# Kernel tuning notes

Hardware: AMD Instinct MI355X
Metric: run time of the kernel (lower is better)

Reference implementation:

```python
import jax, jax.numpy as jnp
import numpy as np

GWIDTH2 = 0.3  # Gaussian bandwidth squared
PNORM = 2


def setup_inputs() -> dict:
    key = jax.random.key(0)
    k1, k2 = jax.random.split(key)
    b, c, h, w = 16, 3, 256, 256
    npro = 32
    x = jax.random.uniform(k1, (b, c, h, w), dtype=jnp.float32)  # pixel values in [0,1]
    P = jax.random.uniform(k2, (npro, c), dtype=jnp.float32)     # p x c prototype pixels
    return {"x": x, "P": P}


def reference(x, P):
    # x: (b, c, h, w); P: (p, c)
    b, c, h, w = x.shape
    # broadcast difference -> (b, p, c, h, w); pnorm=2 distance over channels
    diff = x[:, None, :, :, :] - P[None, :, :, None, None]
    normsp = jnp.sum(diff ** PNORM, axis=2) ** (1.0 / PNORM)  # (b, p, h, w)
    expo = jnp.exp(-normsp / (2.0 * GWIDTH2))
    Y = jnp.sum(expo, axis=(2, 3))  # (b, p)
    return Y / (h * w)
```

## Files before the change

### kernel.cpp

```cpp
#include <hip/hip_runtime.h>


#define NPRO    32
#define HW      65536
#define THREADS 256
#define BPB     32
#define KITER   (HW / (BPB * THREADS * 4))

__global__ __launch_bounds__(THREADS) void soft_count_kernel(
    const float* __restrict__ x, const float* __restrict__ P,
    float* __restrict__ out)
{
    __shared__ float sP[NPRO * 3];
    __shared__ float sred[4][NPRO];

    const int tid = threadIdx.x;
    if (tid < NPRO * 3) sP[tid] = P[tid];
    __syncthreads();

    const int b   = blockIdx.x / BPB;
    const int blk = blockIdx.x % BPB;

    const float* xr = x + (size_t)b * 3 * HW;
    const float* xg = xr + HW;
    const float* xb = xr + 2 * HW;

    float acc[NPRO];
#pragma unroll
    for (int p = 0; p < NPRO; ++p) acc[p] = 0.0f;

    const int base = blk * (THREADS * 4 * KITER);

#pragma unroll
    for (int k = 0; k < KITER; ++k) {
        const int idx = base + k * (THREADS * 4) + tid * 4;
        const float4 r4 = *(const float4*)(xr + idx);
        const float4 g4 = *(const float4*)(xg + idx);
        const float4 b4 = *(const float4*)(xb + idx);
        const float rr[4] = {r4.x, r4.y, r4.z, r4.w};
        const float gg[4] = {g4.x, g4.y, g4.z, g4.w};
        const float bb[4] = {b4.x, b4.y, b4.z, b4.w};

#pragma unroll
        for (int p = 0; p < NPRO; ++p) {
            const float p0 = sP[p * 3 + 0];
            const float p1 = sP[p * 3 + 1];
            const float p2 = sP[p * 3 + 2];
            float s = 0.0f;
#pragma unroll
            for (int j = 0; j < 4; ++j) {
                const float d0 = rr[j] - p0;
                const float d1 = gg[j] - p1;
                const float d2 = bb[j] - p2;
                const float n2 = d0 * d0 + d1 * d1 + d2 * d2;
                const float nrm = sqrtf(n2);
                s += __expf(nrm * (-1.0f / 0.6f));
            }
            acc[p] += s;
        }
    }

    const int lane = tid & 63;
    const int wv   = tid >> 6;
#pragma unroll
    for (int p = 0; p < NPRO; ++p) {
        float v = acc[p];
#pragma unroll
        for (int off = 32; off >= 1; off >>= 1)
            v += __shfl_down(v, off, 64);
        if (lane == 0) sred[wv][p] = v;
    }
    __syncthreads();

    if (tid < NPRO) {
        const float v = sred[0][tid] + sred[1][tid] + sred[2][tid] + sred[3][tid];
        atomicAdd(&out[b * NPRO + tid], v * (1.0f / (float)HW));
    }
}

__global__ void zero_out_kernel(float* out, int n) {
    const int i = blockIdx.x * blockDim.x + threadIdx.x;
    if (i < n) out[i] = 0.0f;
}

extern "C" void kernel_launch(void* const* d_in, const int* in_sizes, int n_in,
                              void* d_out, int out_size, void* d_ws, size_t ws_size,
                              hipStream_t stream) {
    const float* x = (const float*)d_in[0];
    const float* P = (const float*)d_in[1];
    float* out = (float*)d_out;

    const int nb = in_sizes[0] / (3 * HW);

    zero_out_kernel<<<(out_size + 255) / 256, 256, 0, stream>>>(out, out_size);
    soft_count_kernel<<<nb * BPB, THREADS, 0, stream>>>(x, P, out);
}
```

Measured before the change: 87.39 us.

## Double grid blocks, use raw sqrt/exp2 intrinsics, memset output instead of zero kernel

```diff
diff --git a/kernel.cpp b/kernel.cpp
--- a/kernel.cpp
+++ b/kernel.cpp
@@ -4,8 +4,7 @@
 #define NPRO    32
 #define HW      65536
 #define THREADS 256
-#define BPB     32
-#define KITER   (HW / (BPB * THREADS * 4))
+#define BPB     64
 
 __global__ __launch_bounds__(THREADS) void soft_count_kernel(
     const float* __restrict__ x, const float* __restrict__ P,
@@ -21,43 +20,35 @@
     const int b   = blockIdx.x / BPB;
     const int blk = blockIdx.x % BPB;
 
-    const float* xr = x + (size_t)b * 3 * HW;
-    const float* xg = xr + HW;
-    const float* xb = xr + 2 * HW;
+    const float* base = x + (size_t)b * 3 * HW;
+    const int idx = blk * (THREADS * 4) + tid * 4;
+
+    const float4 r4 = *(const float4*)(base + idx);
+    const float4 g4 = *(const float4*)(base + HW + idx);
+    const float4 b4 = *(const float4*)(base + 2 * HW + idx);
+    const float rr[4] = {r4.x, r4.y, r4.z, r4.w};
+    const float gg[4] = {g4.x, g4.y, g4.z, g4.w};
+    const float bb[4] = {b4.x, b4.y, b4.z, b4.w};
+
+    const float C = -2.4044917f;
 
     float acc[NPRO];
 #pragma unroll
-    for (int p = 0; p < NPRO; ++p) acc[p] = 0.0f;
-
-    const int base = blk * (THREADS * 4 * KITER);
-
+    for (int p = 0; p < NPRO; ++p) {
+        const float p0 = sP[p * 3 + 0];
+        const float p1 = sP[p * 3 + 1];
+        const float p2 = sP[p * 3 + 2];
+        float s = 0.0f;
 #pragma unroll
-    for (int k = 0; k < KITER; ++k) {
-        const int idx = base + k * (THREADS * 4) + tid * 4;
-        const float4 r4 = *(const float4*)(xr + idx);
-        const float4 g4 = *(const float4*)(xg + idx);
-        const float4 b4 = *(const float4*)(xb + idx);
-        const float rr[4] = {r4.x, r4.y, r4.z, r4.w};
-        const float gg[4] = {g4.x, g4.y, g4.z, g4.w};
-        const float bb[4] = {b4.x, b4.y, b4.z, b4.w};
-
-#pragma unroll
-        for (int p = 0; p < NPRO; ++p) {
-            const float p0 = sP[p * 3 + 0];
-            const float p1 = sP[p * 3 + 1];
-            const float p2 = sP[p * 3 + 2];
-            float s = 0.0f;
-#pragma unroll
-            for (int j = 0; j < 4; ++j) {
-                const float d0 = rr[j] - p0;
-                const float d1 = gg[j] - p1;
-                const float d2 = bb[j] - p2;
-                const float n2 = d0 * d0 + d1 * d1 + d2 * d2;
-                const float nrm = sqrtf(n2);
-                s += __expf(nrm * (-1.0f / 0.6f));
-            }
-            acc[p] += s;
+        for (int j = 0; j < 4; ++j) {
+            const float d0 = rr[j] - p0;
+            const float d1 = gg[j] - p1;
+            const float d2 = bb[j] - p2;
+            const float n2 = fmaf(d2, d2, fmaf(d1, d1, d0 * d0));
+            const float nrm = __builtin_amdgcn_sqrtf(n2);
+            s += __builtin_amdgcn_exp2f(nrm * C);
         }
+        acc[p] = s;
     }
 
     const int lane = tid & 63;
@@ -78,11 +69,6 @@
     }
 }
 
-__global__ void zero_out_kernel(float* out, int n) {
-    const int i = blockIdx.x * blockDim.x + threadIdx.x;
-    if (i < n) out[i] = 0.0f;
-}
-
 extern "C" void kernel_launch(void* const* d_in, const int* in_sizes, int n_in,
                               void* d_out, int out_size, void* d_ws, size_t ws_size,
                               hipStream_t stream) {
@@ -92,6 +78,6 @@
 
     const int nb = in_sizes[0] / (3 * HW);
 
-    zero_out_kernel<<<(out_size + 255) / 256, 256, 0, stream>>>(out, out_size);
+    hipMemsetAsync(out, 0, (size_t)out_size * sizeof(float), stream);
     soft_count_kernel<<<nb * BPB, THREADS, 0, stream>>>(x, P, out);
 }
```

After: 77.46 us. 11.4% less time.
